# Kernel optimization log

Hardware: AMD Instinct MI355X
Metric: run time of the kernel (lower is better)

## Reference

```python
import jax, jax.numpy as jnp
import numpy as np

GAMMA = 0.1
BATCH, NUM_SV, DIM = 8192, 8192, 256


def setup_inputs() -> dict:
    key = jax.random.key(0)
    k1, k2, k3 = jax.random.split(key, 3)
    x = jax.random.normal(k1, (BATCH, DIM), dtype=jnp.float32)
    support_vectors = jax.random.normal(k2, (NUM_SV, DIM), dtype=jnp.float32)
    dual_coefficients = jax.random.normal(k3, (NUM_SV,), dtype=jnp.float32)
    return {"x": x, "support_vectors": support_vectors, "dual_coefficients": dual_coefficients}


def reference(x, support_vectors, dual_coefficients):
    # Squared Euclidean distance via the GEMM expansion (same math as
    # sum((x[:,None,:]-sv[None,:,:])**2, -1) without the (B, S, D) intermediate).
    x_sq = jnp.sum(x * x, axis=-1, keepdims=True)            # (B, 1)
    sv_sq = jnp.sum(support_vectors * support_vectors, -1)   # (S,)
    cross = jnp.einsum('bd,sd->bs', x, support_vectors)      # (B, S)
    sq_dist = jnp.maximum(x_sq + sv_sq[None, :] - 2.0 * cross, 0.0)
    kernel_matrix = jnp.exp(-GAMMA * sq_dist)                # (B, S)
    return jnp.einsum('bs,s->b', kernel_matrix, dual_coefficients)
```

## Files before the change

kernel.cpp:

```cpp
#include <hip/hip_runtime.h>

#define BATCH 8192
#define NUM_SV 8192
#define DIM 256
#define GAMMA 0.1f
#define LOG2E 1.4426950408889634f
#define ALPHA 0.53715827f

#define BM 256
#define BS 256
#define BK 32
#define SCHUNK 8
#define NST 4
#define NKC (DIM / BK)
#define TILE_F16 8192

typedef _Float16 f16;
typedef __attribute__((ext_vector_type(8))) _Float16 f16x8;
typedef __attribute__((ext_vector_type(16))) float f32x16;

__device__ __forceinline__ void gload_lds16(const f16* g, f16* l) {
  __builtin_amdgcn_global_load_lds((const __attribute__((address_space(1))) void*)g,
                                   (__attribute__((address_space(3))) void*)l, 16, 0, 0);
}

__global__ __launch_bounds__(256)
void svm_prep(const float* __restrict__ x, const float* __restrict__ sv,
              const float* __restrict__ dual,
              f16* __restrict__ x16, f16* __restrict__ sv16,
              float* __restrict__ xg, float* __restrict__ dcp) {
  const int id = blockIdx.x * 256 + threadIdx.x;
  const bool isx = id < (BATCH * DIM / 8);
  const int lid = isx ? id : id - (BATCH * DIM / 8);
  const int row = lid >> 5;
  const int k0  = (lid & 31) << 3;

  const float* src = (isx ? x : sv) + (size_t)row * DIM + k0;
  float4 u = *(const float4*)(src);
  float4 v = *(const float4*)(src + 4);

  float sq = u.x*u.x + u.y*u.y + u.z*u.z + u.w*u.w
           + v.x*v.x + v.y*v.y + v.z*v.z + v.w*v.w;
  #pragma unroll
  for (int m = 1; m <= 16; m <<= 1) sq += __shfl_xor(sq, m, 32);
  if ((lid & 31) == 0) {
    float g = -(GAMMA * LOG2E) * sq;
    if (isx) xg[row] = g;
    else     dcp[row] = dual[row] * __builtin_amdgcn_exp2f(g);
  }

  f16x8 h;
  h[0] = (f16)(ALPHA * u.x); h[1] = (f16)(ALPHA * u.y);
  h[2] = (f16)(ALPHA * u.z); h[3] = (f16)(ALPHA * u.w);
  h[4] = (f16)(ALPHA * v.x); h[5] = (f16)(ALPHA * v.y);
  h[6] = (f16)(ALPHA * v.z); h[7] = (f16)(ALPHA * v.w);

  const int bt = row >> 8;
  const int r  = row & 255;
  const int kc = k0 >> 5;
  const int c  = (k0 >> 3) & 3;
  f16* dst = (isx ? x16 : sv16) + (size_t)(bt * NKC + kc) * TILE_F16 + (c * 256 + r) * 8;
  *(f16x8*)dst = h;
}

__global__ __launch_bounds__(512, 2)
void svm_main(const f16* __restrict__ x16, const f16* __restrict__ sv16,
              const float* __restrict__ dcp, float* __restrict__ partial) {
  __shared__ f16 lds[2][2 * TILE_F16];

  const int tid = threadIdx.x;
  const int w   = tid >> 6;
  const int l   = tid & 63;
  const int lr  = l & 31;
  const int lh  = l >> 5;
  const int wb  = w >> 1;
  const int wn  = w & 1;
  const int sch = blockIdx.x;
  const int bt  = blockIdx.y;
  const int stile0 = sch * NST;

  f32x16 acc[2][4];
  float ctr[2][16];
  #pragma unroll
  for (int m = 0; m < 2; ++m) {
    #pragma unroll
    for (int n = 0; n < 4; ++n)
      #pragma unroll
      for (int r = 0; r < 16; ++r) acc[m][n][r] = 0.f;
    #pragma unroll
    for (int r = 0; r < 16; ++r) ctr[m][r] = 0.f;
  }

  auto stage = [&](int bb, int stile, int kc) {
    const f16* xb = x16  + (size_t)(bt * NKC + kc) * TILE_F16;
    const f16* sb = sv16 + (size_t)(stile * NKC + kc) * TILE_F16;
    #pragma unroll
    for (int j = 0; j < 4; ++j) {
      const int r = w * 4 + j;
      const f16* src = (r < 16) ? (xb + r * 512 + l * 8)
                                : (sb + (r - 16) * 512 + l * 8);
      gload_lds16(src, &lds[bb][r * 512]);
    }
  };

  auto compute = [&](int bb) {
    const f16* buf = lds[bb];
    f16x8 af[2][2], bf[4][2];
    #pragma unroll
    for (int m = 0; m < 2; ++m)
      #pragma unroll
      for (int ks = 0; ks < 2; ++ks)
        af[m][ks] = *(const f16x8*)&buf[((ks * 2 + lh) * 256 + wb * 64 + m * 32 + lr) * 8];
    #pragma unroll
    for (int n = 0; n < 4; ++n)
      #pragma unroll
      for (int ks = 0; ks < 2; ++ks)
        bf[n][ks] = *(const f16x8*)&buf[TILE_F16 + ((ks * 2 + lh) * 256 + wn * 128 + n * 32 + lr) * 8];
    #pragma unroll
    for (int m = 0; m < 2; ++m)
      #pragma unroll
      for (int n = 0; n < 4; ++n) {
        acc[m][n] = __builtin_amdgcn_mfma_f32_32x32x16_f16(af[m][0], bf[n][0], acc[m][n], 0, 0, 0);
        acc[m][n] = __builtin_amdgcn_mfma_f32_32x32x16_f16(af[m][1], bf[n][1], acc[m][n], 0, 0, 0);
      }
  };

  stage(0, stile0, 0);
  int cur = 0;
  for (int t = 0; t < NST * NKC; ++t) {
    __syncthreads();
    if (t + 1 < NST * NKC)
      stage(cur ^ 1, stile0 + ((t + 1) >> 3), (t + 1) & 7);
    compute(cur);
    if ((t & 7) == 7) {
      const int stile = stile0 + (t >> 3);
      #pragma unroll
      for (int n = 0; n < 4; ++n) {
        const float dv = dcp[stile * 256 + wn * 128 + n * 32 + lr];
        #pragma unroll
        for (int m = 0; m < 2; ++m) {
          #pragma unroll
          for (int r = 0; r < 16; ++r) {
            ctr[m][r] = fmaf(__builtin_amdgcn_exp2f(acc[m][n][r]), dv, ctr[m][r]);
            acc[m][n][r] = 0.f;
          }
        }
      }
    }
    cur ^= 1;
  }

  #pragma unroll
  for (int m = 0; m < 2; ++m)
    #pragma unroll
    for (int r = 0; r < 16; ++r) {
      float v = ctr[m][r];
      v += __shfl_xor(v, 1, 64);
      v += __shfl_xor(v, 2, 64);
      v += __shfl_xor(v, 4, 64);
      v += __shfl_xor(v, 8, 64);
      v += __shfl_xor(v, 16, 64);
      ctr[m][r] = v;
    }

  __syncthreads();
  float* red = (float*)&lds[0][0];
  if (lr == 0) {
    #pragma unroll
    for (int m = 0; m < 2; ++m)
      #pragma unroll
      for (int r = 0; r < 16; ++r) {
        const int rl = wb * 64 + m * 32 + (r & 3) + 8 * (r >> 2) + 4 * lh;
        red[wn * 256 + rl] = ctr[m][r];
      }
  }
  __syncthreads();
  if (tid < 256)
    partial[(size_t)sch * BATCH + bt * 256 + tid] = red[tid] + red[256 + tid];
}

__global__ __launch_bounds__(256)
void svm_reduce(const float* __restrict__ partial, const float* __restrict__ xg,
                float* __restrict__ out) {
  const int b = blockIdx.x * 256 + threadIdx.x;
  float s = 0.f;
  #pragma unroll
  for (int c = 0; c < SCHUNK; ++c) s += partial[(size_t)c * BATCH + b];
  out[b] = __builtin_amdgcn_exp2f(xg[b]) * s;
}

extern "C" void kernel_launch(void* const* d_in, const int* in_sizes, int n_in,
                              void* d_out, int out_size, void* d_ws, size_t ws_size,
                              hipStream_t stream) {
  const float* x    = (const float*)d_in[0];
  const float* sv   = (const float*)d_in[1];
  const float* dual = (const float*)d_in[2];
  float* out = (float*)d_out;

  f16*   x16     = (f16*)d_ws;
  f16*   sv16    = x16 + (size_t)BATCH * DIM;
  float* xg      = (float*)(sv16 + (size_t)NUM_SV * DIM);
  float* dcp     = xg + BATCH;
  float* partial = dcp + NUM_SV;

  svm_prep<<<(BATCH + NUM_SV) * DIM / 8 / 256, 256, 0, stream>>>(x, sv, dual, x16, sv16, xg, dcp);
  svm_main<<<dim3(SCHUNK, BATCH / BM), 512, 0, stream>>>(x16, sv16, dcp, partial);
  svm_reduce<<<BATCH / 256, 256, 0, stream>>>(partial, xg, out);
}
```

Measured before the change: 54.26 us.

## Triple-buffer LDS pipeline with explicit vmcnt waits and MFMA priority

Moves the main GEMM loop from a double-buffered LDS scheme with full __syncthreads to a three-buffer ring. Loads are issued two steps ahead, and each step waits with a partial s_waitcnt vmcnt plus a raw s_barrier, so global-to-LDS traffic can overlap more MFMA work. It also preloads the dual coefficients into registers up front, interleaves fragment loads with MFMAs per k-step, and raises wave priority around the MFMA bursts. In exchange, LDS use grows by half, which may limit the two-blocks-per-CU occupancy. The hand-tuned waitcnt values also tie correctness to the exact number of outstanding loads per stage.

```diff
diff --git a/kernel.cpp b/kernel.cpp
--- a/kernel.cpp
+++ b/kernel.cpp
@@ -7,12 +7,10 @@
 #define LOG2E 1.4426950408889634f
 #define ALPHA 0.53715827f
 
-#define BM 256
-#define BS 256
-#define BK 32
 #define SCHUNK 8
 #define NST 4
-#define NKC (DIM / BK)
+#define NKC 8
+#define NITER (NST * NKC)
 #define TILE_F16 8192
 
 typedef _Float16 f16;
@@ -66,7 +64,7 @@
 __global__ __launch_bounds__(512, 2)
 void svm_main(const f16* __restrict__ x16, const f16* __restrict__ sv16,
               const float* __restrict__ dcp, float* __restrict__ partial) {
-  __shared__ f16 lds[2][2 * TILE_F16];
+  __shared__ f16 lds[3][2 * TILE_F16];
 
   const int tid = threadIdx.x;
   const int w   = tid >> 6;
@@ -79,19 +77,14 @@
   const int bt  = blockIdx.y;
   const int stile0 = sch * NST;
 
-  f32x16 acc[2][4];
-  float ctr[2][16];
-  #pragma unroll
-  for (int m = 0; m < 2; ++m) {
+  float dvv[NST][4];
+  #pragma unroll
+  for (int st = 0; st < NST; ++st)
     #pragma unroll
     for (int n = 0; n < 4; ++n)
-      #pragma unroll
-      for (int r = 0; r < 16; ++r) acc[m][n][r] = 0.f;
-    #pragma unroll
-    for (int r = 0; r < 16; ++r) ctr[m][r] = 0.f;
-  }
-
-  auto stage = [&](int bb, int stile, int kc) {
+      dvv[st][n] = dcp[(stile0 + st) * 256 + wn * 128 + n * 32 + lr];
+
+  auto stage = [&](f16* dst, int stile, int kc) {
     const f16* xb = x16  + (size_t)(bt * NKC + kc) * TILE_F16;
     const f16* sb = sv16 + (size_t)(stile * NKC + kc) * TILE_F16;
     #pragma unroll
@@ -99,55 +92,77 @@
       const int r = w * 4 + j;
       const f16* src = (r < 16) ? (xb + r * 512 + l * 8)
                                 : (sb + (r - 16) * 512 + l * 8);
-      gload_lds16(src, &lds[bb][r * 512]);
+      gload_lds16(src, dst + r * 512);
     }
   };
 
-  auto compute = [&](int bb) {
-    const f16* buf = lds[bb];
-    f16x8 af[2][2], bf[4][2];
+  float ctr[2][16];
+  #pragma unroll
+  for (int m = 0; m < 2; ++m)
+    #pragma unroll
+    for (int r = 0; r < 16; ++r) ctr[m][r] = 0.f;
+
+  stage(&lds[0][0], stile0, 0);
+  stage(&lds[1][0], stile0, 1);
+  int ib = 0;
+
+  #pragma unroll
+  for (int st = 0; st < NST; ++st) {
+    f32x16 acc[2][4];
     #pragma unroll
     for (int m = 0; m < 2; ++m)
       #pragma unroll
-      for (int ks = 0; ks < 2; ++ks)
-        af[m][ks] = *(const f16x8*)&buf[((ks * 2 + lh) * 256 + wb * 64 + m * 32 + lr) * 8];
-    #pragma unroll
-    for (int n = 0; n < 4; ++n)
-      #pragma unroll
-      for (int ks = 0; ks < 2; ++ks)
-        bf[n][ks] = *(const f16x8*)&buf[TILE_F16 + ((ks * 2 + lh) * 256 + wn * 128 + n * 32 + lr) * 8];
-    #pragma unroll
-    for (int m = 0; m < 2; ++m)
-      #pragma unroll
-      for (int n = 0; n < 4; ++n) {
-        acc[m][n] = __builtin_amdgcn_mfma_f32_32x32x16_f16(af[m][0], bf[n][0], acc[m][n], 0, 0, 0);
-        acc[m][n] = __builtin_amdgcn_mfma_f32_32x32x16_f16(af[m][1], bf[n][1], acc[m][n], 0, 0, 0);
+      for (int n = 0; n < 4; ++n)
+        #pragma unroll
+        for (int r = 0; r < 16; ++r) acc[m][n][r] = 0.f;
+
+    for (int kc = 0; kc < NKC; ++kc) {
+      __builtin_amdgcn_sched_barrier(0);
+      if (st < NST - 1 || kc < NKC - 1)
+        asm volatile("s_waitcnt vmcnt(4)" ::: "memory");
+      else
+        asm volatile("s_waitcnt vmcnt(0)" ::: "memory");
+      __builtin_amdgcn_s_barrier();
+      __builtin_amdgcn_sched_barrier(0);
+
+      const int t2 = st * NKC + kc + 2;
+      int ib2 = ib + 2; if (ib2 >= 3) ib2 -= 3;
+      if (t2 < NITER)
+        stage(&lds[ib2][0], stile0 + (t2 >> 3), t2 & 7);
+
+      const f16* buf = &lds[ib][0];
+      #pragma unroll
+      for (int ks = 0; ks < 2; ++ks) {
+        const int ko = (ks * 2 + lh) * 256;
+        f16x8 a0 = *(const f16x8*)&buf[(ko + wb * 64 +  0 + lr) * 8];
+        f16x8 a1 = *(const f16x8*)&buf[(ko + wb * 64 + 32 + lr) * 8];
+        f16x8 b0 = *(const f16x8*)&buf[TILE_F16 + (ko + wn * 128 +  0 + lr) * 8];
+        f16x8 b1 = *(const f16x8*)&buf[TILE_F16 + (ko + wn * 128 + 32 + lr) * 8];
+        f16x8 b2 = *(const f16x8*)&buf[TILE_F16 + (ko + wn * 128 + 64 + lr) * 8];
+        f16x8 b3 = *(const f16x8*)&buf[TILE_F16 + (ko + wn * 128 + 96 + lr) * 8];
+        __builtin_amdgcn_s_setprio(1);
+        acc[0][0] = __builtin_amdgcn_mfma_f32_32x32x16_f16(a0, b0, acc[0][0], 0, 0, 0);
+        acc[0][1] = __builtin_amdgcn_mfma_f32_32x32x16_f16(a0, b1, acc[0][1], 0, 0, 0);
+        acc[0][2] = __builtin_amdgcn_mfma_f32_32x32x16_f16(a0, b2, acc[0][2], 0, 0, 0);
+        acc[0][3] = __builtin_amdgcn_mfma_f32_32x32x16_f16(a0, b3, acc[0][3], 0, 0, 0);
+        acc[1][0] = __builtin_amdgcn_mfma_f32_32x32x16_f16(a1, b0, acc[1][0], 0, 0, 0);
+        acc[1][1] = __builtin_amdgcn_mfma_f32_32x32x16_f16(a1, b1, acc[1][1], 0, 0, 0);
+        acc[1][2] = __builtin_amdgcn_mfma_f32_32x32x16_f16(a1, b2, acc[1][2], 0, 0, 0);
+        acc[1][3] = __builtin_amdgcn_mfma_f32_32x32x16_f16(a1, b3, acc[1][3], 0, 0, 0);
+        __builtin_amdgcn_s_setprio(0);
       }
-  };
-
-  stage(0, stile0, 0);
-  int cur = 0;
-  for (int t = 0; t < NST * NKC; ++t) {
-    __syncthreads();
-    if (t + 1 < NST * NKC)
-      stage(cur ^ 1, stile0 + ((t + 1) >> 3), (t + 1) & 7);
-    compute(cur);
-    if ((t & 7) == 7) {
-      const int stile = stile0 + (t >> 3);
-      #pragma unroll
-      for (int n = 0; n < 4; ++n) {
-        const float dv = dcp[stile * 256 + wn * 128 + n * 32 + lr];
+      ib = ib + 1; if (ib >= 3) ib -= 3;
+    }
+
+    #pragma unroll
+    for (int n = 0; n < 4; ++n) {
+      const float dv = dvv[st][n];
+      #pragma unroll
+      for (int m = 0; m < 2; ++m)
         #pragma unroll
-        for (int m = 0; m < 2; ++m) {
-          #pragma unroll
-          for (int r = 0; r < 16; ++r) {
-            ctr[m][r] = fmaf(__builtin_amdgcn_exp2f(acc[m][n][r]), dv, ctr[m][r]);
-            acc[m][n][r] = 0.f;
-          }
-        }
-      }
-    }
-    cur ^= 1;
+        for (int r = 0; r < 16; ++r)
+          ctr[m][r] = fmaf(__builtin_amdgcn_exp2f(acc[m][n][r]), dv, ctr[m][r]);
+    }
   }
 
   #pragma unroll
@@ -204,6 +219,6 @@
   float* partial = dcp + NUM_SV;
 
   svm_prep<<<(BATCH + NUM_SV) * DIM / 8 / 256, 256, 0, stream>>>(x, sv, dual, x16, sv16, xg, dcp);
-  svm_main<<<dim3(SCHUNK, BATCH / BM), 512, 0, stream>>>(x16, sv16, dcp, partial);
+  svm_main<<<dim3(SCHUNK, BATCH / 256), 512, 0, stream>>>(x16, sv16, dcp, partial);
   svm_reduce<<<BATCH / 256, 256, 0, stream>>>(partial, xg, out);
 }
```

New measurement: 107.3 us. +97.8%, slower.

## Restructure GEMM main loop into four-phase ping-pong pipeline with BK=64 halves

Applied to the files above, without the earlier changes.

Changes the fp16 tile layout to 64-wide K chunks split into row halves, and replaces the simple double-buffered loop with a four-phase schedule. Each phase issues LDS fragment reads, one async global-to-LDS half-tile load, and then a barrier-fenced batch of MFMAs with raised priority. Explicit vmcnt waits keep two tiles in flight. The dual coefficients are also cached in LDS once per block. The aim is to hide global-load and LDS latency behind MFMA work and cut the barriers per FLOP, at the cost of fragile hand-tuned waitcnt and barrier ordering.

```diff
diff --git a/kernel.cpp b/kernel.cpp
--- a/kernel.cpp
+++ b/kernel.cpp
@@ -7,13 +7,10 @@
 #define LOG2E 1.4426950408889634f
 #define ALPHA 0.53715827f
 
-#define BM 256
-#define BS 256
-#define BK 32
 #define SCHUNK 8
 #define NST 4
-#define NKC (DIM / BK)
-#define TILE_F16 8192
+#define NITER 16
+#define HALF_F16 8192
 
 typedef _Float16 f16;
 typedef __attribute__((ext_vector_type(8))) _Float16 f16x8;
@@ -55,18 +52,25 @@
   h[4] = (f16)(ALPHA * v.x); h[5] = (f16)(ALPHA * v.y);
   h[6] = (f16)(ALPHA * v.z); h[7] = (f16)(ALPHA * v.w);
 
-  const int bt = row >> 8;
-  const int r  = row & 255;
-  const int kc = k0 >> 5;
-  const int c  = (k0 >> 3) & 3;
-  f16* dst = (isx ? x16 : sv16) + (size_t)(bt * NKC + kc) * TILE_F16 + (c * 256 + r) * 8;
+  const int tile  = row >> 8;
+  const int r     = row & 255;
+  const int half  = r >> 7;
+  const int rfrag = (r >> 5) & 3;
+  const int rowin = r & 31;
+  const int kt    = k0 >> 6;
+  const int ks    = (k0 >> 4) & 3;
+  const int kch   = (k0 >> 3) & 1;
+  f16* dst = (isx ? x16 : sv16)
+           + (size_t)(((tile * 4 + kt) * 2 + half) * HALF_F16)
+           + ks * 2048 + rfrag * 512 + kch * 256 + rowin * 8;
   *(f16x8*)dst = h;
 }
 
 __global__ __launch_bounds__(512, 2)
 void svm_main(const f16* __restrict__ x16, const f16* __restrict__ sv16,
               const float* __restrict__ dcp, float* __restrict__ partial) {
-  __shared__ f16 lds[2][2 * TILE_F16];
+  __shared__ f16 lds[2][2][2][HALF_F16];
+  __shared__ float dcpl[NST * 256];
 
   const int tid = threadIdx.x;
   const int w   = tid >> 6;
@@ -79,6 +83,59 @@
   const int bt  = blockIdx.y;
   const int stile0 = sch * NST;
 
+  *(float2*)&dcpl[tid * 2] = *(const float2*)&dcp[stile0 * 256 + tid * 2];
+
+  auto stageA = [&](int ut, int half) {
+    const f16* src = x16 + (size_t)(((bt * 4 + (ut & 3)) * 2 + half) * HALF_F16) + tid * 8;
+    f16* dst = &lds[ut & 1][0][half][tid * 8];
+    gload_lds16(src, dst);
+    gload_lds16(src + 4096, dst + 4096);
+  };
+  auto stageB = [&](int ut, int half) {
+    const f16* src = sv16 + (size_t)((((stile0 + (ut >> 2)) * 4 + (ut & 3)) * 2 + half) * HALF_F16) + tid * 8;
+    f16* dst = &lds[ut & 1][1][half][tid * 8];
+    gload_lds16(src, dst);
+    gload_lds16(src + 4096, dst + 4096);
+  };
+
+#define LOAD_A(ksh)                                                          \
+  do {                                                                       \
+    const f16* Ab = &lds[u & 1][0][wb >> 1][(wb & 1) * 1024 + l * 8];        \
+    af[0][0] = *(const f16x8*)&Ab[((ksh) * 2 + 0) * 2048];                   \
+    af[0][1] = *(const f16x8*)&Ab[((ksh) * 2 + 1) * 2048];                   \
+    af[1][0] = *(const f16x8*)&Ab[((ksh) * 2 + 0) * 2048 + 512];             \
+    af[1][1] = *(const f16x8*)&Ab[((ksh) * 2 + 1) * 2048 + 512];             \
+  } while (0)
+
+#define LOAD_B(nfh, ksh)                                                     \
+  do {                                                                       \
+    const f16* Bb = &lds[u & 1][1][wn][(nfh) * 1024 + l * 8];                \
+    bf[0][0] = *(const f16x8*)&Bb[((ksh) * 2 + 0) * 2048];                   \
+    bf[0][1] = *(const f16x8*)&Bb[((ksh) * 2 + 1) * 2048];                   \
+    bf[1][0] = *(const f16x8*)&Bb[((ksh) * 2 + 0) * 2048 + 512];             \
+    bf[1][1] = *(const f16x8*)&Bb[((ksh) * 2 + 1) * 2048 + 512];             \
+  } while (0)
+
+#define PH_SYNC                                                              \
+  do {                                                                       \
+    __builtin_amdgcn_s_barrier();                                            \
+    asm volatile("s_waitcnt lgkmcnt(0)" ::: "memory");                       \
+    __builtin_amdgcn_sched_barrier(0);                                       \
+  } while (0)
+
+#define MFMA1(m, nf, ksl)                                                    \
+  acc[m][nf] = __builtin_amdgcn_mfma_f32_32x32x16_f16(af[m][ksl], bf[(nf) & 1][ksl], acc[m][nf], 0, 0, 0)
+
+#define MFMA_PH(nfh)                                                         \
+  do {                                                                       \
+    __builtin_amdgcn_s_setprio(1);                                           \
+    MFMA1(0, (nfh) * 2 + 0, 0); MFMA1(0, (nfh) * 2 + 1, 0);                  \
+    MFMA1(1, (nfh) * 2 + 0, 0); MFMA1(1, (nfh) * 2 + 1, 0);                  \
+    MFMA1(0, (nfh) * 2 + 0, 1); MFMA1(0, (nfh) * 2 + 1, 1);                  \
+    MFMA1(1, (nfh) * 2 + 0, 1); MFMA1(1, (nfh) * 2 + 1, 1);                  \
+    __builtin_amdgcn_s_setprio(0);                                           \
+  } while (0)
+
   f32x16 acc[2][4];
   float ctr[2][16];
   #pragma unroll
@@ -91,64 +148,53 @@
     for (int r = 0; r < 16; ++r) ctr[m][r] = 0.f;
   }
 
-  auto stage = [&](int bb, int stile, int kc) {
-    const f16* xb = x16  + (size_t)(bt * NKC + kc) * TILE_F16;
-    const f16* sb = sv16 + (size_t)(stile * NKC + kc) * TILE_F16;
-    #pragma unroll
-    for (int j = 0; j < 4; ++j) {
-      const int r = w * 4 + j;
-      const f16* src = (r < 16) ? (xb + r * 512 + l * 8)
-                                : (sb + (r - 16) * 512 + l * 8);
-      gload_lds16(src, &lds[bb][r * 512]);
-    }
-  };
-
-  auto compute = [&](int bb) {
-    const f16* buf = lds[bb];
-    f16x8 af[2][2], bf[4][2];
-    #pragma unroll
-    for (int m = 0; m < 2; ++m)
+  stageA(0, 0); stageA(0, 1); stageB(0, 0); stageB(0, 1);
+  stageA(1, 0); stageA(1, 1); stageB(1, 0); stageB(1, 1);
+  asm volatile("s_waitcnt vmcnt(8) lgkmcnt(0)" ::: "memory");
+  __builtin_amdgcn_s_barrier();
+
+  f16x8 af[2][2], bf[2][2];
+
+  #pragma unroll 1
+  for (int u = 0; u < NITER; ++u) {
+    LOAD_A(0); LOAD_B(0, 0);
+    if (u >= 1 && u < NITER - 1) stageA(u + 1, 1);
+    PH_SYNC; MFMA_PH(0);
+    __builtin_amdgcn_s_barrier();
+
+    LOAD_B(1, 0);
+    if (u >= 1 && u < NITER - 1) stageB(u + 1, 0);
+    PH_SYNC; MFMA_PH(1);
+    __builtin_amdgcn_s_barrier();
+
+    LOAD_A(1); LOAD_B(1, 1);
+    if (u >= 1 && u < NITER - 1) stageB(u + 1, 1);
+    PH_SYNC; MFMA_PH(1);
+    __builtin_amdgcn_s_barrier();
+
+    LOAD_B(0, 1);
+    if (u < NITER - 2) stageA(u + 2, 0);
+    PH_SYNC; MFMA_PH(0);
+    asm volatile("s_waitcnt vmcnt(2)" ::: "memory");
+    __builtin_amdgcn_s_barrier();
+
+    if ((u & 3) == 3) {
+      const int st = u >> 2;
       #pragma unroll
-      for (int ks = 0; ks < 2; ++ks)
-        af[m][ks] = *(const f16x8*)&buf[((ks * 2 + lh) * 256 + wb * 64 + m * 32 + lr) * 8];
-    #pragma unroll
-    for (int n = 0; n < 4; ++n)
-      #pragma unroll
-      for (int ks = 0; ks < 2; ++ks)
-        bf[n][ks] = *(const f16x8*)&buf[TILE_F16 + ((ks * 2 + lh) * 256 + wn * 128 + n * 32 + lr) * 8];
-    #pragma unroll
-    for (int m = 0; m < 2; ++m)
-      #pragma unroll
-      for (int n = 0; n < 4; ++n) {
-        acc[m][n] = __builtin_amdgcn_mfma_f32_32x32x16_f16(af[m][0], bf[n][0], acc[m][n], 0, 0, 0);
-        acc[m][n] = __builtin_amdgcn_mfma_f32_32x32x16_f16(af[m][1], bf[n][1], acc[m][n], 0, 0, 0);
-      }
-  };
-
-  stage(0, stile0, 0);
-  int cur = 0;
-  for (int t = 0; t < NST * NKC; ++t) {
-    __syncthreads();
-    if (t + 1 < NST * NKC)
-      stage(cur ^ 1, stile0 + ((t + 1) >> 3), (t + 1) & 7);
-    compute(cur);
-    if ((t & 7) == 7) {
-      const int stile = stile0 + (t >> 3);
-      #pragma unroll
-      for (int n = 0; n < 4; ++n) {
-        const float dv = dcp[stile * 256 + wn * 128 + n * 32 + lr];
+      for (int nf = 0; nf < 4; ++nf) {
+        const float dv = dcpl[st * 256 + wn * 128 + nf * 32 + lr];
         #pragma unroll
-        for (int m = 0; m < 2; ++m) {
+        for (int m = 0; m < 2; ++m)
           #pragma unroll
           for (int r = 0; r < 16; ++r) {
-            ctr[m][r] = fmaf(__builtin_amdgcn_exp2f(acc[m][n][r]), dv, ctr[m][r]);
-            acc[m][n][r] = 0.f;
+            ctr[m][r] = fmaf(__builtin_amdgcn_exp2f(acc[m][nf][r]), dv, ctr[m][r]);
+            acc[m][nf][r] = 0.f;
           }
-        }
       }
     }
-    cur ^= 1;
-  }
+  }
+
+  asm volatile("s_waitcnt vmcnt(0)" ::: "memory");
 
   #pragma unroll
   for (int m = 0; m < 2; ++m)
@@ -164,7 +210,7 @@
     }
 
   __syncthreads();
-  float* red = (float*)&lds[0][0];
+  float* red = (float*)&lds[0][0][0][0];
   if (lr == 0) {
     #pragma unroll
     for (int m = 0; m < 2; ++m)
@@ -204,6 +250,6 @@
   float* partial = dcp + NUM_SV;
 
   svm_prep<<<(BATCH + NUM_SV) * DIM / 8 / 256, 256, 0, stream>>>(x, sv, dual, x16, sv16, xg, dcp);
-  svm_main<<<dim3(SCHUNK, BATCH / BM), 512, 0, stream>>>(x16, sv16, dcp, partial);
+  svm_main<<<dim3(SCHUNK, BATCH / 256), 512, 0, stream>>>(x16, sv16, dcp, partial);
   svm_reduce<<<BATCH / 256, 256, 0, stream>>>(partial, xg, out);
 }
```

Result: no change. 54.67 us (+0.8%).
